# Performance work log

Hardware: AMD Instinct MI355X
Metric: run time of the kernel (lower is better)

The kernel has to match this reference:

```python
import jax, jax.numpy as jnp
import numpy as np

B, T_ENC, T_DEC = 16, 256, 64
N_MEL = 80
ENC_DIM = 512
ATTN_RNN_DIM = 1024
DEC_RNN_DIM = 1024
PRENET_DIM = 256
ATTN_DIM = 128
LOC_FILTERS = 32
LOC_KERNEL = 31


def setup_inputs() -> dict:
    key = jax.random.key(0)
    ks = jax.random.split(key, 32)
    s = 0.02
    inp = {
        "memory": jax.random.normal(ks[0], (B, T_ENC, ENC_DIM), jnp.float32),
        "decoder_inputs": jax.random.normal(ks[1], (B, N_MEL, T_DEC), jnp.float32),
        "memory_lengths": jax.random.randint(ks[2], (B,), T_ENC // 2, T_ENC + 1, jnp.int32),
        # prenet
        "prenet_W1": jax.random.normal(ks[3], (PRENET_DIM, N_MEL), jnp.float32) * s,
        "prenet_b1": jnp.zeros((PRENET_DIM,), jnp.float32),
        "prenet_W2": jax.random.normal(ks[4], (PRENET_DIM, PRENET_DIM), jnp.float32) * s,
        "prenet_b2": jnp.zeros((PRENET_DIM,), jnp.float32),
        # attention LSTMCell: input = prenet_dim + enc_dim
        "attn_rnn_Wih": jax.random.normal(ks[5], (4 * ATTN_RNN_DIM, PRENET_DIM + ENC_DIM), jnp.float32) * s,
        "attn_rnn_Whh": jax.random.normal(ks[6], (4 * ATTN_RNN_DIM, ATTN_RNN_DIM), jnp.float32) * s,
        "attn_rnn_bih": jnp.zeros((4 * ATTN_RNN_DIM,), jnp.float32),
        "attn_rnn_bhh": jnp.zeros((4 * ATTN_RNN_DIM,), jnp.float32),
        # attention projections (bias-free, Tacotron2 style)
        "query_W": jax.random.normal(ks[7], (ATTN_DIM, ATTN_RNN_DIM), jnp.float32) * s,
        "mem_W": jax.random.normal(ks[8], (ATTN_DIM, ENC_DIM), jnp.float32) * s,
        "loc_conv_W": jax.random.normal(ks[9], (LOC_FILTERS, 2, LOC_KERNEL), jnp.float32) * s,
        "loc_dense_W": jax.random.normal(ks[10], (ATTN_DIM, LOC_FILTERS), jnp.float32) * s,
        "attn_v": jax.random.normal(ks[11], (1, ATTN_DIM), jnp.float32) * s,
        # decoder LSTMCell: input = attn_rnn_dim + enc_dim
        "dec_rnn_Wih": jax.random.normal(ks[12], (4 * DEC_RNN_DIM, ATTN_RNN_DIM + ENC_DIM), jnp.float32) * s,
        "dec_rnn_Whh": jax.random.normal(ks[13], (4 * DEC_RNN_DIM, DEC_RNN_DIM), jnp.float32) * s,
        "dec_rnn_bih": jnp.zeros((4 * DEC_RNN_DIM,), jnp.float32),
        "dec_rnn_bhh": jnp.zeros((4 * DEC_RNN_DIM,), jnp.float32),
        # output heads
        "proj_W": jax.random.normal(ks[14], (N_MEL, DEC_RNN_DIM + ENC_DIM), jnp.float32) * s,
        "proj_b": jnp.zeros((N_MEL,), jnp.float32),
        "gate_W": jax.random.normal(ks[15], (1, DEC_RNN_DIM + ENC_DIM), jnp.float32) * s,
        "gate_b": jnp.zeros((1,), jnp.float32),
    }
    return inp


def _lstm_cell(x, h, c, Wih, Whh, bih, bhh):
    gates = x @ Wih.T + bih + h @ Whh.T + bhh  # [B, 4H]
    i, f, g, o = jnp.split(gates, 4, axis=-1)
    c2 = jax.nn.sigmoid(f) * c + jax.nn.sigmoid(i) * jnp.tanh(g)
    h2 = jax.nn.sigmoid(o) * jnp.tanh(c2)
    return h2, c2


def _decoder_forward(memory, decoder_inputs, memory_lengths,
                     prenet_W1, prenet_b1, prenet_W2, prenet_b2,
                     attn_rnn_Wih, attn_rnn_Whh, attn_rnn_bih, attn_rnn_bhh,
                     query_W, mem_W, loc_conv_W, loc_dense_W, attn_v,
                     dec_rnn_Wih, dec_rnn_Whh, dec_rnn_bih, dec_rnn_bhh,
                     proj_W, proj_b, gate_W, gate_b):
    b, t_enc, _ = memory.shape
    t_dec = decoder_inputs.shape[2]
    # parse_decoder_inputs: [B,80,T] -> [T,B,80]; prepend go frame
    frames = jnp.transpose(decoder_inputs, (2, 0, 1))  # [T,B,80]
    go = jnp.zeros((1, b, N_MEL), frames.dtype)
    frames = jnp.concatenate([go, frames], axis=0)  # [T+1,B,80]
    # prenet (dropout disabled for determinism)
    pre = jax.nn.relu(frames @ prenet_W1.T + prenet_b1)
    pre = jax.nn.relu(pre @ prenet_W2.T + prenet_b2)  # [T+1,B,256]
    pre = pre[:-1]  # steps use frames 0..T-1

    processed_memory = memory @ mem_W.T  # [B,T_enc,128]
    pad_mask = jnp.arange(t_enc)[None, :] >= memory_lengths[:, None]  # [B,T_enc] True=pad

    pad = (LOC_KERNEL - 1) // 2

    def step(carry, x_t):
        (ah, ac, dh, dc, aw, aw_cum, ctx) = carry
        cell_in = jnp.concatenate([x_t, ctx], axis=-1)
        ah, ac = _lstm_cell(cell_in, ah, ac, attn_rnn_Wih, attn_rnn_Whh, attn_rnn_bih, attn_rnn_bhh)
        # location-sensitive attention
        awc = jnp.stack([aw, aw_cum], axis=1)  # [B,2,T_enc]
        loc = jax.lax.conv_general_dilated(
            awc, loc_conv_W, window_strides=(1,), padding=[(pad, pad)],
            dimension_numbers=("NCH", "OIH", "NCH"))  # [B,32,T_enc]
        loc = jnp.transpose(loc, (0, 2, 1)) @ loc_dense_W.T  # [B,T_enc,128]
        query = (ah @ query_W.T)[:, None, :]  # [B,1,128]
        energies = jnp.squeeze(jnp.tanh(query + processed_memory + loc) @ attn_v.T, -1)  # [B,T_enc]
        energies = jnp.where(pad_mask, -1e9, energies)
        aw = jax.nn.softmax(energies, axis=1)
        ctx = jnp.einsum("bt,btd->bd", aw, memory)
        aw_cum = aw_cum + aw
        dec_in = jnp.concatenate([ah, ctx], axis=-1)
        dh, dc = _lstm_cell(dec_in, dh, dc, dec_rnn_Wih, dec_rnn_Whh, dec_rnn_bih, dec_rnn_bhh)
        dhc = jnp.concatenate([dh, ctx], axis=-1)
        mel = dhc @ proj_W.T + proj_b  # [B,80]
        gate = jnp.squeeze(dhc @ gate_W.T + gate_b, -1)  # [B]
        return (ah, ac, dh, dc, aw, aw_cum, ctx), (mel, gate, aw)

    z = jnp.zeros
    carry0 = (z((b, ATTN_RNN_DIM)), z((b, ATTN_RNN_DIM)),
              z((b, DEC_RNN_DIM)), z((b, DEC_RNN_DIM)),
              z((b, t_enc)), z((b, t_enc)), z((b, ENC_DIM)))
    _, (mels, gates, aligns) = jax.lax.scan(step, carry0, pre)
    # parse_decoder_outputs
    mel_outputs = jnp.transpose(mels, (1, 2, 0))  # [B,80,T_dec]
    gate_outputs = jnp.transpose(gates, (1, 0))  # [B,T_dec]
    alignments = jnp.transpose(aligns, (1, 0, 2))  # [B,T_dec,T_enc]
    return mel_outputs, gate_outputs, alignments


def reference(memory, decoder_inputs, memory_lengths,
              prenet_W1, prenet_b1, prenet_W2, prenet_b2,
              attn_rnn_Wih, attn_rnn_Whh, attn_rnn_bih, attn_rnn_bhh,
              query_W, mem_W, loc_conv_W, loc_dense_W, attn_v,
              dec_rnn_Wih, dec_rnn_Whh, dec_rnn_bih, dec_rnn_bhh,
              proj_W, proj_b, gate_W, gate_b):
    return _decoder_forward(memory, decoder_inputs, memory_lengths,
                            prenet_W1, prenet_b1, prenet_W2, prenet_b2,
                            attn_rnn_Wih, attn_rnn_Whh, attn_rnn_bih, attn_rnn_bhh,
                            query_W, mem_W, loc_conv_W, loc_dense_W, attn_v,
                            dec_rnn_Wih, dec_rnn_Whh, dec_rnn_bih, dec_rnn_bhh,
                            proj_W, proj_b, gate_W, gate_b)
```

## Files before the change

kernel.cpp:

```cpp
#include <hip/hip_runtime.h>

typedef __attribute__((ext_vector_type(8))) short short8;
typedef __attribute__((ext_vector_type(4))) float f32x4;
typedef unsigned short u16;
typedef unsigned int u32;
typedef unsigned long long u64;


static constexpr size_t OFF_WFA   = 0;
static constexpr size_t OFF_WFD   = 14680064;
static constexpr size_t OFF_PREF  = 35651584;
static constexpr size_t OFF_QWF   = 36175872;
static constexpr size_t OFF_MWT   = 36438016;
static constexpr size_t OFF_BA    = 36700160;
static constexpr size_t OFF_BD    = 36716544;
static constexpr size_t OFF_PM    = 36732928;
static constexpr size_t OFF_CTXF  = 38830080;
static constexpr size_t OFF_DHF   = 40960000;
static constexpr size_t OFF_AHFD  = 45219840;
static constexpr size_t OFF_CTXFD = 47349760;
static constexpr size_t OFF_DHFD  = 48414720;
static constexpr size_t OFF_BAR   = 50544640;
static constexpr size_t OFF_END   = 50548736;

__device__ __forceinline__ float sigmf(float x) { return 1.f / (1.f + expf(-x)); }
__device__ __forceinline__ float tanh_fast(float x) {
  float e2 = __expf(2.f * x);
  return 1.f - 2.f / (e2 + 1.f);
}
__device__ __forceinline__ u16 f2bf(float f) {
  u32 u = __float_as_uint(f);
  return (u16)((u + 0x7FFFu + ((u >> 16) & 1u)) >> 16);
}
__device__ __forceinline__ float bf2f(u16 x) { return __uint_as_float(((u32)x) << 16); }

__device__ __forceinline__ short8 ld_frag(const void* p) {
  return *(const short8*)p;
}
__device__ __forceinline__ short8 ld_frag_nt(const void* p) {
  const u64* q = (const u64*)p;
  u64 lo = __builtin_nontemporal_load(q);
  u64 hi = __builtin_nontemporal_load(q + 1);
  union { u64 q2[2]; short8 s; } u;
  u.q2[0] = lo; u.q2[1] = hi;
  return u.s;
}

__device__ __forceinline__ void st_u16_agent(u16* p, u16 v) {
  __hip_atomic_store(p, v, __ATOMIC_RELAXED, __HIP_MEMORY_SCOPE_AGENT);
}
__device__ __forceinline__ void st_f32_agent(float* p, float v) {
  __hip_atomic_store(p, v, __ATOMIC_RELAXED, __HIP_MEMORY_SCOPE_AGENT);
}
__device__ __forceinline__ void st_u64_agent(u64* p, u64 v) {
  __hip_atomic_store(p, v, __ATOMIC_RELAXED, __HIP_MEMORY_SCOPE_AGENT);
}
__device__ __forceinline__ u32 ld_u32_agent(const u32* p) {
  return __hip_atomic_load(p, __ATOMIC_RELAXED, __HIP_MEMORY_SCOPE_AGENT);
}
__device__ __forceinline__ void st_u32_agent(u32* p, u32 v) {
  __hip_atomic_store(p, v, __ATOMIC_RELAXED, __HIP_MEMORY_SCOPE_AGENT);
}

template <int SLP>
__device__ __forceinline__ void wait16(const u32* F, u32 target, int th) {
  if (th < 64) {
    const u32* pf = F + (th & 15) * 16;
    for (;;) {
      u32 v = ld_u32_agent(pf);
      if (__all(v >= target)) break;
      __builtin_amdgcn_s_sleep(SLP);
    }
  }
  __syncthreads();
}

__global__ void k_wfrag(const float* __restrict__ Wih, const float* __restrict__ Whh,
                        char* __restrict__ dst, int NT, int Kih) {
  int idx = blockIdx.x * 256 + threadIdx.x;
  int l = idx & 63;
  int st = idx >> 6;
  int s = st % NT, tile = st / NT;
  int r = l & 15, kg = l >> 4;
  int j = (r >> 2) * 1024 + tile * 4 + (r & 3);
  int k0 = s * 32 + kg * 8;
  const float* src = (k0 < Kih) ? (Wih + (size_t)j * Kih + k0)
                                : (Whh + (size_t)j * 1024 + (k0 - Kih));
  short8 v;
#pragma unroll
  for (int e = 0; e < 8; ++e) v[e] = (short)f2bf(src[e]);
  *(short8*)(dst + (size_t)idx * 16) = v;
}

__global__ void k_qwfrag(const float* __restrict__ qW, char* __restrict__ dst) {
  int idx = blockIdx.x * 256 + threadIdx.x;
  int l = idx & 63, tile = idx >> 6;
  int dt = tile >> 5, kt = tile & 31;
  int j = dt * 16 + (l & 15);
  int k0 = kt * 32 + (l >> 4) * 8;
  short8 v;
#pragma unroll
  for (int e = 0; e < 8; ++e) v[e] = (short)f2bf(qW[j * 1024 + k0 + e]);
  *(short8*)(dst + (size_t)idx * 16) = v;
}

__global__ void k_smallprep(const float* __restrict__ memW,
                            const float* __restrict__ abih, const float* __restrict__ abhh,
                            const float* __restrict__ dbih, const float* __restrict__ dbhh,
                            char* __restrict__ wsb) {
  int idx = blockIdx.x * 256 + threadIdx.x;
  if (idx < 65536) {
    int k = idx >> 7, d = idx & 127;
    ((float*)(wsb + OFF_MWT))[idx] = memW[d * 512 + k];
  } else if (idx < 69632) {
    int j = idx - 65536;
    ((float*)(wsb + OFF_BA))[j] = abih[j] + abhh[j];
  } else if (idx < 73728) {
    int j = idx - 69632;
    ((float*)(wsb + OFF_BD))[j] = dbih[j] + dbhh[j];
  }
}

__global__ void k_prenet(const float* __restrict__ dec_in,
                         const float* __restrict__ W1, const float* __restrict__ b1,
                         const float* __restrict__ W2, const float* __restrict__ b2,
                         char* __restrict__ wsb) {
  int s = blockIdx.x, b = blockIdx.y, th = threadIdx.x;
  __shared__ float frame[80];
  __shared__ float h1[256];
  if (th < 80) frame[th] = (s == 0) ? 0.f : dec_in[(b * 80 + th) * 64 + (s - 1)];
  __syncthreads();
  float a = b1[th];
  const float* w1r = W1 + th * 80;
  for (int m = 0; m < 80; ++m) a += w1r[m] * frame[m];
  h1[th] = fmaxf(a, 0.f);
  __syncthreads();
  float a2 = b2[th];
  const float* w2r = W2 + th * 256;
  for (int i = 0; i < 256; ++i) a2 += w2r[i] * h1[i];
  float pre = fmaxf(a2, 0.f);
  int k = th;
  ((u16*)(wsb + OFF_PREF))[(((size_t)s * 8 + (k >> 5)) * 64 + ((k >> 3) & 3) * 16 + b) * 8 + (k & 7)] = f2bf(pre);
}

__global__ void k_pm(const float* __restrict__ memory, char* __restrict__ wsb) {
  int bk = blockIdx.x, th = threadIdx.x;
  int b = bk >> 4, t0 = (bk & 15) * 16;
  __shared__ float mrow[16 * 512];
  for (int i = 0; i < 8; ++i) {
    int fi4 = i * 256 + th;
    int tl = fi4 >> 7, k4 = (fi4 & 127) << 2;
    *(float4*)&mrow[tl * 512 + k4] =
        *(const float4*)&memory[((size_t)(b * 256 + t0 + tl)) * 512 + k4];
  }
  __syncthreads();
  int d = th & 127, tl0 = th >> 7;
  float acc[8] = {};
  const float* mWT = (const float*)(wsb + OFF_MWT);
  float* pmw = (float*)(wsb + OFF_PM);
  for (int k = 0; k < 512; ++k) {
    float w = mWT[k * 128 + d];
#pragma unroll
    for (int i = 0; i < 8; ++i) acc[i] += w * mrow[(tl0 + i * 2) * 512 + k];
  }
  for (int i = 0; i < 8; ++i)
    pmw[((size_t)(b * 256 + t0 + tl0 + i * 2)) * 128 + d] = acc[i];
}

struct KParams {
  const float* memory;
  const int* mlen;
  const float* convW;
  const float* ldW;
  const float* attnv;
  const float* projW;
  const float* projb;
  const float* gateW;
  const float* gateb;
  char* wsb;
  float* out;
};

__global__ void __launch_bounds__(512, 1) k_main(KParams p) {
  const int th = threadIdx.x;
  const int bk = blockIdx.x;
  char* wsb = p.wsb;
  const int l = th & 63, w = th >> 6;
  u32* Af = (u32*)(wsb + OFF_BAR);
  u32* Df = (u32*)(wsb + OFF_BAR + 1024);
  u32* Bf = (u32*)(wsb + OFF_BAR + 2048);

  __shared__ float smC[4608];
  __shared__ float s2q[128], s2v[128];
  __shared__ u16 s_convF[8192];
  __shared__ u16 s_pack[512];
  __shared__ float s_e[256], s3wr[4];
  __shared__ float s1cw[1984];
  __shared__ float s_aw[256], s_awc[256];
  __shared__ float smW[4096];
  __shared__ u16 sp[1024];

  const float* pm = (const float*)(wsb + OFF_PM);

  if (bk < 16) {
    for (int i = th; i < 1984; i += 512) s1cw[i] = p.convW[i];
    for (int i = th; i < 4096; i += 512) ((u32*)s_convF)[i] = 0u;
    if (th < 128) s2v[th] = p.attnv[th];
    if (th < 256) { s_aw[th] = 0.f; s_awc[th] = 0.f; }
  }
  int lenB = 0;
  if (bk < 16) lenB = p.mlen[bk];

  short8 ldwB[8];
  if (bk < 16) {
    int kg = l >> 4, dcol = l & 15;
#pragma unroll
    for (int dt = 0; dt < 8; ++dt) {
      short8 v;
#pragma unroll
      for (int e = 0; e < 8; ++e)
        v[e] = (short)f2bf(p.ldW[(dt * 16 + dcol) * 32 + kg * 8 + e]);
      ldwB[dt] = v;
    }
  }
  __syncthreads();

  if (bk >= 16 && bk < 32) {
    const int i = bk - 16;
    const char* wfa = wsb + OFF_WFA;
    const int tI0 = i * 16 + w * 2;
    float bA[2][4], cA2[2] = {0.f, 0.f};
    {
      const float* ba = (const float*)(wsb + OFF_BA);
#pragma unroll
      for (int pq = 0; pq < 2; ++pq) {
        int idx = l * 2 + pq, lu = idx >> 4;
        int u = i * 64 + w * 8 + lu;
#pragma unroll
        for (int g = 0; g < 4; ++g) bA[pq][g] = ba[g * 1024 + u];
      }
    }
    f32x4 acc0, acc1;
    auto EARLY = [&](int t) {
      acc0 = f32x4{0.f, 0.f, 0.f, 0.f};
      acc1 = f32x4{0.f, 0.f, 0.f, 0.f};
      for (int e = 0; e < 40; ++e) {
        int s = (e < 8) ? e : (24 + (e - 8));
        const char* bsrc = (e < 8)
            ? wsb + OFF_PREF + (((size_t)t * 8 + s) * 64 + l) * 16
            : wsb + OFF_AHFD + (((size_t)t * 32 + (s - 24)) * 64 + l) * 16;
        short8 bv = ld_frag(bsrc);
        short8 a0 = *(const short8*)(wfa + (((size_t)tI0 * 56 + s) * 64 + l) * 16);
        short8 a1 = *(const short8*)(wfa + (((size_t)(tI0 + 1) * 56 + s) * 64 + l) * 16);
        acc0 = __builtin_amdgcn_mfma_f32_16x16x32_bf16(a0, bv, acc0, 0, 0, 0);
        acc1 = __builtin_amdgcn_mfma_f32_16x16x32_bf16(a1, bv, acc1, 0, 0, 0);
      }
    };
    EARLY(0);
    for (int t = 0; t < 64; ++t) {
      wait16<1>(Bf, (u32)t, th);
#pragma unroll
      for (int s = 8; s < 24; ++s) {
        short8 bv = ld_frag(wsb + OFF_CTXFD + (((size_t)t * 16 + (s - 8)) * 64 + l) * 16);
        short8 a0 = *(const short8*)(wfa + (((size_t)tI0 * 56 + s) * 64 + l) * 16);
        short8 a1 = *(const short8*)(wfa + (((size_t)(tI0 + 1) * 56 + s) * 64 + l) * 16);
        acc0 = __builtin_amdgcn_mfma_f32_16x16x32_bf16(a0, bv, acc0, 0, 0, 0);
        acc1 = __builtin_amdgcn_mfma_f32_16x16x32_bf16(a1, bv, acc1, 0, 0, 0);
      }
      {
        float* myW = smW + w * 512;
#pragma unroll
        for (int r4 = 0; r4 < 4; ++r4) {
          myW[((l >> 4) * 4 + r4) * 16 + (l & 15)] = acc0[r4];
          myW[256 + ((l >> 4) * 4 + r4) * 16 + (l & 15)] = acc1[r4];
        }
      }
      __syncthreads();
      {
        const float* myW = smW + w * 512;
        u16* myP = sp + w * 128;
#pragma unroll
        for (int pq = 0; pq < 2; ++pq) {
          int idx = l * 2 + pq, lu = idx >> 4, b = idx & 15;
          int rt = lu >> 2, uoff = lu & 3;
          float gi = myW[rt * 256 + (0 * 4 + uoff) * 16 + b] + bA[pq][0];
          float gf = myW[rt * 256 + (1 * 4 + uoff) * 16 + b] + bA[pq][1];
          float gg = myW[rt * 256 + (2 * 4 + uoff) * 16 + b] + bA[pq][2];
          float go = myW[rt * 256 + (3 * 4 + uoff) * 16 + b] + bA[pq][3];
          float c2 = sigmf(gf) * cA2[pq] + sigmf(gi) * tanhf(gg);
          float h2 = sigmf(go) * tanhf(c2);
          cA2[pq] = c2;
          myP[b * 8 + lu] = f2bf(h2);
        }
      }
      __syncthreads();
      if (l < 16) {
        const u64* src = (const u64*)(sp + w * 128) + l * 2;
        int slab = i * 8 + w;
        u64* dst = (u64*)(wsb + OFF_AHFD + ((size_t)(t + 1) * 32 + (slab >> 2)) * 1024 +
                          ((size_t)((slab & 3) * 16 + l)) * 16);
        st_u64_agent(dst, src[0]);
        st_u64_agent(dst + 1, src[1]);
      }
      __syncthreads();
      if (th == 0) st_u32_agent(Af + i * 16, (u32)(t + 1));
      if (t < 63) {
        wait16<1>(Af, (u32)(t + 1), th);
        EARLY(t + 1);
      }
    }
  } else if (bk >= 32 && bk < 48) {
    const int j = bk - 32;
    const char* wfd = wsb + OFF_WFD;
    const int tI0 = j * 16 + w * 2;
    float bD[2][4], cD2[2] = {0.f, 0.f};
    {
      const float* bd = (const float*)(wsb + OFF_BD);
#pragma unroll
      for (int pq = 0; pq < 2; ++pq) {
        int idx = l * 2 + pq, lu = idx >> 4;
        int u = j * 64 + w * 8 + lu;
#pragma unroll
        for (int g = 0; g < 4; ++g) bD[pq][g] = bd[g * 1024 + u];
      }
    }
    for (int t = 1; t <= 64; ++t) {
      wait16<2>(Af, (u32)t, th);
      wait16<2>(Bf, (u32)t, th);
      if (t >= 2) wait16<2>(Df, (u32)(t - 1), th);
      f32x4 acc0 = {0.f, 0.f, 0.f, 0.f}, acc1 = {0.f, 0.f, 0.f, 0.f};
      for (int s = 0; s < 80; ++s) {
        const char* bsrc;
        if (s < 32)      bsrc = wsb + OFF_AHFD + (((size_t)t * 32 + s) * 64 + l) * 16;
        else if (s < 48) bsrc = wsb + OFF_CTXFD + (((size_t)t * 16 + (s - 32)) * 64 + l) * 16;
        else             bsrc = wsb + OFF_DHFD + (((size_t)(t - 1) * 32 + (s - 48)) * 64 + l) * 16;
        short8 bv = ld_frag_nt(bsrc);
        short8 a0 = ld_frag_nt(wfd + (((size_t)tI0 * 80 + s) * 64 + l) * 16);
        short8 a1 = ld_frag_nt(wfd + (((size_t)(tI0 + 1) * 80 + s) * 64 + l) * 16);
        acc0 = __builtin_amdgcn_mfma_f32_16x16x32_bf16(a0, bv, acc0, 0, 0, 0);
        acc1 = __builtin_amdgcn_mfma_f32_16x16x32_bf16(a1, bv, acc1, 0, 0, 0);
      }
      {
        float* myW = smW + w * 512;
#pragma unroll
        for (int r4 = 0; r4 < 4; ++r4) {
          myW[((l >> 4) * 4 + r4) * 16 + (l & 15)] = acc0[r4];
          myW[256 + ((l >> 4) * 4 + r4) * 16 + (l & 15)] = acc1[r4];
        }
      }
      __syncthreads();
      {
        const float* myW = smW + w * 512;
        u16* myP = sp + w * 128;
        float* dhf = (float*)(wsb + OFF_DHF);
#pragma unroll
        for (int pq = 0; pq < 2; ++pq) {
          int idx = l * 2 + pq, lu = idx >> 4, b = idx & 15;
          int rt = lu >> 2, uoff = lu & 3;
          float gi = myW[rt * 256 + (0 * 4 + uoff) * 16 + b] + bD[pq][0];
          float gf = myW[rt * 256 + (1 * 4 + uoff) * 16 + b] + bD[pq][1];
          float gg = myW[rt * 256 + (2 * 4 + uoff) * 16 + b] + bD[pq][2];
          float go = myW[rt * 256 + (3 * 4 + uoff) * 16 + b] + bD[pq][3];
          float c2 = sigmf(gf) * cD2[pq] + sigmf(gi) * tanhf(gg);
          float h2 = sigmf(go) * tanhf(c2);
          cD2[pq] = c2;
          int u = j * 64 + w * 8 + lu;
          st_f32_agent(dhf + ((size_t)t * 1024 + u) * 16 + b, h2);
          myP[b * 8 + lu] = f2bf(h2);
        }
      }
      __syncthreads();
      if (l < 16) {
        const u64* src = (const u64*)(sp + w * 128) + l * 2;
        int slab = j * 8 + w;
        u64* dst = (u64*)(wsb + OFF_DHFD + ((size_t)t * 32 + (slab >> 2)) * 1024 +
                          ((size_t)((slab & 3) * 16 + l)) * 16);
        st_u64_agent(dst, src[0]);
        st_u64_agent(dst + 1, src[1]);
      }
      __syncthreads();
      if (th == 0) st_u32_agent(Df + j * 16, (u32)t);
    }
  } else if (bk < 16) {
    const int b = bk;
    for (int t = 0; t < 64; ++t) {
      {
        int jmax = (lenB + 15) >> 4;
        for (int jj = 0; jj < jmax; ++jj) {
          int idx = jj * 512 + th, tt = idx >> 5, f = idx & 31;
          float a = 0.f;
          const float* w0 = s1cw + f * 62;
#pragma unroll
          for (int kk = 0; kk < 31; ++kk) {
            int pos = tt + kk - 15;
            bool ok = (pos >= 0 && pos < 256);
            float awv = ok ? s_aw[pos] : 0.f;
            float awcv = ok ? s_awc[pos] : 0.f;
            a += awv * w0[kk] + awcv * w0[31 + kk];
          }
          s_convF[(tt >> 4) * 512 + ((f >> 3) * 16 + (tt & 15)) * 8 + (f & 7)] = f2bf(a);
        }
      }
      wait16<1>(Af, (u32)(t + 1), th);
      {
        f32x4 qacc = {0.f, 0.f, 0.f, 0.f};
        const char* qwf = wsb + OFF_QWF;
#pragma unroll 4
        for (int kt = 0; kt < 32; ++kt) {
          short8 av = *(const short8*)(qwf + (((size_t)w * 32 + kt) * 64 + l) * 16);
          short8 bv = ld_frag(wsb + OFF_AHFD + ((size_t)(t + 1) * 32 + kt) * 1024 +
                              ((size_t)(l >> 4) * 16 + b) * 16);
          qacc = __builtin_amdgcn_mfma_f32_16x16x32_bf16(av, bv, qacc, 0, 0, 0);
        }
        if ((l & 15) == 0) {
          int r0 = (l >> 4) * 4;
          s2q[w * 16 + r0]     = qacc[0];
          s2q[w * 16 + r0 + 1] = qacc[1];
          s2q[w * 16 + r0 + 2] = qacc[2];
          s2q[w * 16 + r0 + 3] = qacc[3];
        }
      }
      __syncthreads();
      {
#pragma unroll
        for (int tl = 0; tl < 2; ++tl) {
          int ttile = w * 2 + tl;
          short8 afc = *(const short8*)&s_convF[ttile * 512 + l * 8];
          int dcol = l & 15;
          float e0 = 0.f, e1 = 0.f, e2 = 0.f, e3 = 0.f;
          const float* pmb = pm + ((size_t)(b * 256 + ttile * 16 + (l >> 4) * 4)) * 128 + dcol;
#pragma unroll
          for (int dt = 0; dt < 8; ++dt) {
            f32x4 S = {0.f, 0.f, 0.f, 0.f};
            S = __builtin_amdgcn_mfma_f32_16x16x32_bf16(afc, ldwB[dt], S, 0, 0, 0);
            int d = dt * 16 + dcol;
            float qd = s2q[d], vd = s2v[d];
            e0 += vd * tanh_fast(qd + pmb[dt * 16 + 0 * 128] + S[0]);
            e1 += vd * tanh_fast(qd + pmb[dt * 16 + 1 * 128] + S[1]);
            e2 += vd * tanh_fast(qd + pmb[dt * 16 + 2 * 128] + S[2]);
            e3 += vd * tanh_fast(qd + pmb[dt * 16 + 3 * 128] + S[3]);
          }
#pragma unroll
          for (int off = 8; off; off >>= 1) {
            e0 += __shfl_xor(e0, off);
            e1 += __shfl_xor(e1, off);
            e2 += __shfl_xor(e2, off);
            e3 += __shfl_xor(e3, off);
          }
          if ((l & 15) == 0) {
            int tb0 = ttile * 16 + (l >> 4) * 4;
            s_e[tb0]     = (tb0     < lenB) ? __expf(e0) : 0.f;
            s_e[tb0 + 1] = (tb0 + 1 < lenB) ? __expf(e1) : 0.f;
            s_e[tb0 + 2] = (tb0 + 2 < lenB) ? __expf(e2) : 0.f;
            s_e[tb0 + 3] = (tb0 + 3 < lenB) ? __expf(e3) : 0.f;
          }
        }
      }
      __syncthreads();
      if (th < 256) {
        float v0 = s_e[th];
#pragma unroll
        for (int off = 32; off; off >>= 1) v0 += __shfl_xor(v0, off);
        if ((th & 63) == 0) s3wr[th >> 6] = v0;
      }
      __syncthreads();
      float rden = 1.f / (s3wr[0] + s3wr[1] + s3wr[2] + s3wr[3]);
      if (th < 256) {
        float a = s_e[th] * rden;
        s_aw[th] = a;
        s_awc[th] += a;
        p.out[82944 + ((size_t)(b * 64 + t)) * 256 + th] = a;
      }
      __syncthreads();
      {
        int dq = th & 127, tg = th >> 7;
        int d0 = dq * 4;
        float a0 = 0.f, a1 = 0.f, a2 = 0.f, a3 = 0.f;
        const float* mb = p.memory + ((size_t)b * 256) * 512 + d0;
        for (int tt = tg; tt < lenB; tt += 4) {
          float4 mv = *(const float4*)(mb + (size_t)tt * 512);
          float aw = s_aw[tt];
          a0 += aw * mv.x; a1 += aw * mv.y; a2 += aw * mv.z; a3 += aw * mv.w;
        }
        smC[tg * 512 + d0]     = a0;
        smC[tg * 512 + d0 + 1] = a1;
        smC[tg * 512 + d0 + 2] = a2;
        smC[tg * 512 + d0 + 3] = a3;
      }
      __syncthreads();
      {
        int d = th;
        float ctxv = smC[d] + smC[512 + d] + smC[1024 + d] + smC[1536 + d];
        st_f32_agent((float*)(wsb + OFF_CTXF) + (size_t)(t + 1) * 8192 + b * 512 + d, ctxv);
        s_pack[d] = f2bf(ctxv);
      }
      __syncthreads();
      if (th < 64) {
        u64 p0 = ((const u64*)s_pack)[th * 2];
        u64 p1 = ((const u64*)s_pack)[th * 2 + 1];
        u64* dst = (u64*)(wsb + OFF_CTXFD + ((size_t)(t + 1) * 16 + (th >> 2)) * 1024 +
                          ((size_t)(th & 3) * 16 + b) * 16);
        st_u64_agent(dst, p0);
        st_u64_agent(dst + 1, p1);
      }
      __syncthreads();
      if (th == 0) st_u32_agent(Bf + b * 16, (u32)(t + 1));
    }
  }

  if (bk >= 48) {
    wait16<64>(Df, 64u, th);
    wait16<64>(Bf, 64u, th);
  } else {
    wait16<4>(Df, 64u, th);
    wait16<4>(Bf, 64u, th);
  }
  {
    int t = bk & 63, pa = bk >> 6;
    const float* dh = (const float*)(wsb + OFF_DHF) + (size_t)(t + 1) * 16384;
    const float* cxt = (const float*)(wsb + OFF_CTXF) + (size_t)(t + 1) * 8192;
    int lim = (pa == 3) ? 336 : 320;
    for (int idx = th; idx < lim; idx += 512) {
      if (idx < 320) {
        int mi = idx >> 4, b = idx & 15, m = pa * 20 + mi;
        const float* wr = p.projW + (size_t)m * 1536;
        const float* cxb = cxt + b * 512;
        float a0 = 0.f, a1 = 0.f;
#pragma unroll 8
        for (int k = 0; k < 1024; k += 2) { a0 += wr[k] * dh[k * 16 + b]; a1 += wr[k + 1] * dh[(k + 1) * 16 + b]; }
#pragma unroll 8
        for (int k = 0; k < 512; k += 2)  { a0 += wr[1024 + k] * cxb[k]; a1 += wr[1025 + k] * cxb[k + 1]; }
        p.out[((size_t)(b * 80 + m)) * 64 + t] = a0 + a1 + p.projb[m];
      } else {
        int b = idx - 320;
        const float* cxb = cxt + b * 512;
        float a0 = 0.f, a1 = 0.f;
#pragma unroll 8
        for (int k = 0; k < 1024; k += 2) { a0 += p.gateW[k] * dh[k * 16 + b]; a1 += p.gateW[k + 1] * dh[(k + 1) * 16 + b]; }
#pragma unroll 8
        for (int k = 0; k < 512; k += 2)  { a0 += p.gateW[1024 + k] * cxb[k]; a1 += p.gateW[1025 + k] * cxb[k + 1]; }
        p.out[81920 + b * 64 + t] = a0 + a1 + p.gateb[0];
      }
    }
  }
}

extern "C" void kernel_launch(void* const* d_in, const int* in_sizes, int n_in,
                              void* d_out, int out_size, void* d_ws, size_t ws_size,
                              hipStream_t stream) {
  (void)in_sizes; (void)n_in; (void)out_size; (void)ws_size;
  const float* memory = (const float*)d_in[0];
  const float* dec_in = (const float*)d_in[1];
  const int*   mlen   = (const int*)d_in[2];
  const float* pW1    = (const float*)d_in[3];
  const float* pb1    = (const float*)d_in[4];
  const float* pW2    = (const float*)d_in[5];
  const float* pb2    = (const float*)d_in[6];
  const float* aWih   = (const float*)d_in[7];
  const float* aWhh   = (const float*)d_in[8];
  const float* abih   = (const float*)d_in[9];
  const float* abhh   = (const float*)d_in[10];
  const float* qW     = (const float*)d_in[11];
  const float* memW   = (const float*)d_in[12];
  const float* convW  = (const float*)d_in[13];
  const float* ldW    = (const float*)d_in[14];
  const float* attnv  = (const float*)d_in[15];
  const float* dWih   = (const float*)d_in[16];
  const float* dWhh   = (const float*)d_in[17];
  const float* dbih   = (const float*)d_in[18];
  const float* dbhh   = (const float*)d_in[19];
  const float* projW  = (const float*)d_in[20];
  const float* projb  = (const float*)d_in[21];
  const float* gateW  = (const float*)d_in[22];
  const float* gateb  = (const float*)d_in[23];
  char* wsb = (char*)d_ws;
  float* out = (float*)d_out;

  hipMemsetAsync(wsb + OFF_AHFD, 0, 32768, stream);
  hipMemsetAsync(wsb + OFF_CTXFD, 0, 16384, stream);
  hipMemsetAsync(wsb + OFF_DHFD, 0, 32768, stream);
  hipMemsetAsync(wsb + OFF_BAR, 0, 4096, stream);

  hipLaunchKernelGGL(k_wfrag, dim3(3584), dim3(256), 0, stream, aWih, aWhh, wsb + OFF_WFA, 56, 768);
  hipLaunchKernelGGL(k_wfrag, dim3(5120), dim3(256), 0, stream, dWih, dWhh, wsb + OFF_WFD, 80, 1536);
  hipLaunchKernelGGL(k_qwfrag, dim3(64), dim3(256), 0, stream, qW, wsb + OFF_QWF);
  hipLaunchKernelGGL(k_smallprep, dim3(288), dim3(256), 0, stream, memW, abih, abhh, dbih, dbhh, wsb);
  hipLaunchKernelGGL(k_prenet, dim3(64, 16), dim3(256), 0, stream, dec_in, pW1, pb1, pW2, pb2, wsb);
  hipLaunchKernelGGL(k_pm, dim3(256), dim3(256), 0, stream, memory, wsb);

  KParams p{memory, mlen, convW, ldW, attnv, projW, projb, gateW, gateb, wsb, out};
  void* args[] = { &p };
  hipLaunchCooperativeKernel((void*)k_main, dim3(256), dim3(512), args, 0, stream);
}
```

Measured before the change: 3.180 ms.

## Spread LSTM cells over twice as many blocks with one MFMA tile per wave

The attention-LSTM and decoder-LSTM recurrences each move from 16 to 32 persistent blocks, with each wave owning a single 16-row weight tile instead of two. The barrier flag arrays are widened and waits over them become 32-flag polls. Block index ranges for the later stages shift to match, and the decoder's nontemporal loads become plain loads. The aim is to halve the serial per-step weight streaming and MFMA chain on each block, at the cost of more inter-block synchronization per timestep.

Result: faster. 2.879 ms (-9.4%).

```diff
diff --git a/kernel.cpp b/kernel.cpp
--- a/kernel.cpp
+++ b/kernel.cpp
@@ -21,7 +21,7 @@
 static constexpr size_t OFF_CTXFD = 47349760;
 static constexpr size_t OFF_DHFD  = 48414720;
 static constexpr size_t OFF_BAR   = 50544640;
-static constexpr size_t OFF_END   = 50548736;
+static constexpr size_t OFF_END   = 50552832;
 
 __device__ __forceinline__ float sigmf(float x) { return 1.f / (1.f + expf(-x)); }
 __device__ __forceinline__ float tanh_fast(float x) {
@@ -37,14 +37,6 @@
 __device__ __forceinline__ short8 ld_frag(const void* p) {
   return *(const short8*)p;
 }
-__device__ __forceinline__ short8 ld_frag_nt(const void* p) {
-  const u64* q = (const u64*)p;
-  u64 lo = __builtin_nontemporal_load(q);
-  u64 hi = __builtin_nontemporal_load(q + 1);
-  union { u64 q2[2]; short8 s; } u;
-  u.q2[0] = lo; u.q2[1] = hi;
-  return u.s;
-}
 
 __device__ __forceinline__ void st_u16_agent(u16* p, u16 v) {
   __hip_atomic_store(p, v, __ATOMIC_RELAXED, __HIP_MEMORY_SCOPE_AGENT);
@@ -66,6 +58,18 @@
 __device__ __forceinline__ void wait16(const u32* F, u32 target, int th) {
   if (th < 64) {
     const u32* pf = F + (th & 15) * 16;
+    for (;;) {
+      u32 v = ld_u32_agent(pf);
+      if (__all(v >= target)) break;
+      __builtin_amdgcn_s_sleep(SLP);
+    }
+  }
+  __syncthreads();
+}
+template <int SLP>
+__device__ __forceinline__ void wait32(const u32* F, u32 target, int th) {
+  if (th < 64) {
+    const u32* pf = F + (th & 31) * 16;
     for (;;) {
       u32 v = ld_u32_agent(pf);
       if (__all(v >= target)) break;
@@ -187,8 +191,8 @@
   char* wsb = p.wsb;
   const int l = th & 63, w = th >> 6;
   u32* Af = (u32*)(wsb + OFF_BAR);
-  u32* Df = (u32*)(wsb + OFF_BAR + 1024);
-  u32* Bf = (u32*)(wsb + OFF_BAR + 2048);
+  u32* Df = (u32*)(wsb + OFF_BAR + 2048);
+  u32* Bf = (u32*)(wsb + OFF_BAR + 4096);
 
   __shared__ float smC[4608];
   __shared__ float s2q[128], s2v[128];
@@ -197,8 +201,8 @@
   __shared__ float s_e[256], s3wr[4];
   __shared__ float s1cw[1984];
   __shared__ float s_aw[256], s_awc[256];
-  __shared__ float smW[4096];
-  __shared__ u16 sp[1024];
+  __shared__ float smW[2048];
+  __shared__ u16 sp[512];
 
   const float* pm = (const float*)(wsb + OFF_PM);
 
@@ -225,35 +229,29 @@
   }
   __syncthreads();
 
-  if (bk >= 16 && bk < 32) {
+  if (bk >= 16 && bk < 48) {
     const int i = bk - 16;
     const char* wfa = wsb + OFF_WFA;
-    const int tI0 = i * 16 + w * 2;
-    float bA[2][4], cA2[2] = {0.f, 0.f};
+    const int tI = i * 8 + w;
+    const int ul = l >> 4, b = l & 15;
+    float bA[4], cA = 0.f;
     {
       const float* ba = (const float*)(wsb + OFF_BA);
-#pragma unroll
-      for (int pq = 0; pq < 2; ++pq) {
-        int idx = l * 2 + pq, lu = idx >> 4;
-        int u = i * 64 + w * 8 + lu;
-#pragma unroll
-        for (int g = 0; g < 4; ++g) bA[pq][g] = ba[g * 1024 + u];
-      }
-    }
-    f32x4 acc0, acc1;
+      int u = tI * 4 + ul;
+#pragma unroll
+      for (int g = 0; g < 4; ++g) bA[g] = ba[g * 1024 + u];
+    }
+    f32x4 acc;
     auto EARLY = [&](int t) {
-      acc0 = f32x4{0.f, 0.f, 0.f, 0.f};
-      acc1 = f32x4{0.f, 0.f, 0.f, 0.f};
+      acc = f32x4{0.f, 0.f, 0.f, 0.f};
       for (int e = 0; e < 40; ++e) {
         int s = (e < 8) ? e : (24 + (e - 8));
         const char* bsrc = (e < 8)
             ? wsb + OFF_PREF + (((size_t)t * 8 + s) * 64 + l) * 16
             : wsb + OFF_AHFD + (((size_t)t * 32 + (s - 24)) * 64 + l) * 16;
         short8 bv = ld_frag(bsrc);
-        short8 a0 = *(const short8*)(wfa + (((size_t)tI0 * 56 + s) * 64 + l) * 16);
-        short8 a1 = *(const short8*)(wfa + (((size_t)(tI0 + 1) * 56 + s) * 64 + l) * 16);
-        acc0 = __builtin_amdgcn_mfma_f32_16x16x32_bf16(a0, bv, acc0, 0, 0, 0);
-        acc1 = __builtin_amdgcn_mfma_f32_16x16x32_bf16(a1, bv, acc1, 0, 0, 0);
+        short8 av = *(const short8*)(wfa + (((size_t)tI * 56 + s) * 64 + l) * 16);
+        acc = __builtin_amdgcn_mfma_f32_16x16x32_bf16(av, bv, acc, 0, 0, 0);
       }
     };
     EARLY(0);
@@ -262,121 +260,95 @@
 #pragma unroll
       for (int s = 8; s < 24; ++s) {
         short8 bv = ld_frag(wsb + OFF_CTXFD + (((size_t)t * 16 + (s - 8)) * 64 + l) * 16);
-        short8 a0 = *(const short8*)(wfa + (((size_t)tI0 * 56 + s) * 64 + l) * 16);
-        short8 a1 = *(const short8*)(wfa + (((size_t)(tI0 + 1) * 56 + s) * 64 + l) * 16);
-        acc0 = __builtin_amdgcn_mfma_f32_16x16x32_bf16(a0, bv, acc0, 0, 0, 0);
-        acc1 = __builtin_amdgcn_mfma_f32_16x16x32_bf16(a1, bv, acc1, 0, 0, 0);
-      }
-      {
-        float* myW = smW + w * 512;
-#pragma unroll
-        for (int r4 = 0; r4 < 4; ++r4) {
-          myW[((l >> 4) * 4 + r4) * 16 + (l & 15)] = acc0[r4];
-          myW[256 + ((l >> 4) * 4 + r4) * 16 + (l & 15)] = acc1[r4];
-        }
-      }
-      __syncthreads();
-      {
-        const float* myW = smW + w * 512;
-        u16* myP = sp + w * 128;
-#pragma unroll
-        for (int pq = 0; pq < 2; ++pq) {
-          int idx = l * 2 + pq, lu = idx >> 4, b = idx & 15;
-          int rt = lu >> 2, uoff = lu & 3;
-          float gi = myW[rt * 256 + (0 * 4 + uoff) * 16 + b] + bA[pq][0];
-          float gf = myW[rt * 256 + (1 * 4 + uoff) * 16 + b] + bA[pq][1];
-          float gg = myW[rt * 256 + (2 * 4 + uoff) * 16 + b] + bA[pq][2];
-          float go = myW[rt * 256 + (3 * 4 + uoff) * 16 + b] + bA[pq][3];
-          float c2 = sigmf(gf) * cA2[pq] + sigmf(gi) * tanhf(gg);
-          float h2 = sigmf(go) * tanhf(c2);
-          cA2[pq] = c2;
-          myP[b * 8 + lu] = f2bf(h2);
-        }
+        short8 av = *(const short8*)(wfa + (((size_t)tI * 56 + s) * 64 + l) * 16);
+        acc = __builtin_amdgcn_mfma_f32_16x16x32_bf16(av, bv, acc, 0, 0, 0);
+      }
+      {
+        float* myW = smW + w * 256;
+#pragma unroll
+        for (int r4 = 0; r4 < 4; ++r4)
+          myW[((l >> 4) * 4 + r4) * 16 + (l & 15)] = acc[r4];
+      }
+      __syncthreads();
+      {
+        const float* myW = smW + w * 256;
+        u16* myP = sp + w * 64;
+        float gi = myW[(0 * 4 + ul) * 16 + b] + bA[0];
+        float gf = myW[(1 * 4 + ul) * 16 + b] + bA[1];
+        float gg = myW[(2 * 4 + ul) * 16 + b] + bA[2];
+        float go = myW[(3 * 4 + ul) * 16 + b] + bA[3];
+        float c2 = sigmf(gf) * cA + sigmf(gi) * tanhf(gg);
+        float h2 = sigmf(go) * tanhf(c2);
+        cA = c2;
+        myP[b * 4 + ul] = f2bf(h2);
       }
       __syncthreads();
       if (l < 16) {
-        const u64* src = (const u64*)(sp + w * 128) + l * 2;
-        int slab = i * 8 + w;
-        u64* dst = (u64*)(wsb + OFF_AHFD + ((size_t)(t + 1) * 32 + (slab >> 2)) * 1024 +
-                          ((size_t)((slab & 3) * 16 + l)) * 16);
-        st_u64_agent(dst, src[0]);
-        st_u64_agent(dst + 1, src[1]);
+        u64 val = ((const u64*)(sp + w * 64))[l];
+        u64* dst = (u64*)(wsb + OFF_AHFD + ((size_t)(t + 1) * 32 + (tI >> 3)) * 1024 +
+                          ((size_t)(((tI >> 1) & 3) * 16 + l)) * 16 + (size_t)(tI & 1) * 8);
+        st_u64_agent(dst, val);
       }
       __syncthreads();
       if (th == 0) st_u32_agent(Af + i * 16, (u32)(t + 1));
       if (t < 63) {
-        wait16<1>(Af, (u32)(t + 1), th);
+        wait32<1>(Af, (u32)(t + 1), th);
         EARLY(t + 1);
       }
     }
-  } else if (bk >= 32 && bk < 48) {
-    const int j = bk - 32;
+  } else if (bk >= 48 && bk < 80) {
+    const int j = bk - 48;
     const char* wfd = wsb + OFF_WFD;
-    const int tI0 = j * 16 + w * 2;
-    float bD[2][4], cD2[2] = {0.f, 0.f};
+    const int tI = j * 8 + w;
+    const int ul = l >> 4, b = l & 15;
+    float bD[4], cD = 0.f;
     {
       const float* bd = (const float*)(wsb + OFF_BD);
-#pragma unroll
-      for (int pq = 0; pq < 2; ++pq) {
-        int idx = l * 2 + pq, lu = idx >> 4;
-        int u = j * 64 + w * 8 + lu;
-#pragma unroll
-        for (int g = 0; g < 4; ++g) bD[pq][g] = bd[g * 1024 + u];
-      }
+      int u = tI * 4 + ul;
+#pragma unroll
+      for (int g = 0; g < 4; ++g) bD[g] = bd[g * 1024 + u];
     }
     for (int t = 1; t <= 64; ++t) {
-      wait16<2>(Af, (u32)t, th);
+      wait32<2>(Af, (u32)t, th);
       wait16<2>(Bf, (u32)t, th);
-      if (t >= 2) wait16<2>(Df, (u32)(t - 1), th);
-      f32x4 acc0 = {0.f, 0.f, 0.f, 0.f}, acc1 = {0.f, 0.f, 0.f, 0.f};
+      if (t >= 2) wait32<2>(Df, (u32)(t - 1), th);
+      f32x4 acc = {0.f, 0.f, 0.f, 0.f};
       for (int s = 0; s < 80; ++s) {
         const char* bsrc;
         if (s < 32)      bsrc = wsb + OFF_AHFD + (((size_t)t * 32 + s) * 64 + l) * 16;
         else if (s < 48) bsrc = wsb + OFF_CTXFD + (((size_t)t * 16 + (s - 32)) * 64 + l) * 16;
         else             bsrc = wsb + OFF_DHFD + (((size_t)(t - 1) * 32 + (s - 48)) * 64 + l) * 16;
-        short8 bv = ld_frag_nt(bsrc);
-        short8 a0 = ld_frag_nt(wfd + (((size_t)tI0 * 80 + s) * 64 + l) * 16);
-        short8 a1 = ld_frag_nt(wfd + (((size_t)(tI0 + 1) * 80 + s) * 64 + l) * 16);
-        acc0 = __builtin_amdgcn_mfma_f32_16x16x32_bf16(a0, bv, acc0, 0, 0, 0);
-        acc1 = __builtin_amdgcn_mfma_f32_16x16x32_bf16(a1, bv, acc1, 0, 0, 0);
-      }
-      {
-        float* myW = smW + w * 512;
-#pragma unroll
-        for (int r4 = 0; r4 < 4; ++r4) {
-          myW[((l >> 4) * 4 + r4) * 16 + (l & 15)] = acc0[r4];
-          myW[256 + ((l >> 4) * 4 + r4) * 16 + (l & 15)] = acc1[r4];
-        }
-      }
-      __syncthreads();
-      {
-        const float* myW = smW + w * 512;
-        u16* myP = sp + w * 128;
-        float* dhf = (float*)(wsb + OFF_DHF);
-#pragma unroll
-        for (int pq = 0; pq < 2; ++pq) {
-          int idx = l * 2 + pq, lu = idx >> 4, b = idx & 15;
-          int rt = lu >> 2, uoff = lu & 3;
-          float gi = myW[rt * 256 + (0 * 4 + uoff) * 16 + b] + bD[pq][0];
-          float gf = myW[rt * 256 + (1 * 4 + uoff) * 16 + b] + bD[pq][1];
-          float gg = myW[rt * 256 + (2 * 4 + uoff) * 16 + b] + bD[pq][2];
-          float go = myW[rt * 256 + (3 * 4 + uoff) * 16 + b] + bD[pq][3];
-          float c2 = sigmf(gf) * cD2[pq] + sigmf(gi) * tanhf(gg);
-          float h2 = sigmf(go) * tanhf(c2);
-          cD2[pq] = c2;
-          int u = j * 64 + w * 8 + lu;
-          st_f32_agent(dhf + ((size_t)t * 1024 + u) * 16 + b, h2);
-          myP[b * 8 + lu] = f2bf(h2);
-        }
+        short8 bv = ld_frag(bsrc);
+        short8 av = *(const short8*)(wfd + (((size_t)tI * 80 + s) * 64 + l) * 16);
+        acc = __builtin_amdgcn_mfma_f32_16x16x32_bf16(av, bv, acc, 0, 0, 0);
+      }
+      {
+        float* myW = smW + w * 256;
+#pragma unroll
+        for (int r4 = 0; r4 < 4; ++r4)
+          myW[((l >> 4) * 4 + r4) * 16 + (l & 15)] = acc[r4];
+      }
+      __syncthreads();
+      {
+        const float* myW = smW + w * 256;
+        u16* myP = sp + w * 64;
+        float gi = myW[(0 * 4 + ul) * 16 + b] + bD[0];
+        float gf = myW[(1 * 4 + ul) * 16 + b] + bD[1];
+        float gg = myW[(2 * 4 + ul) * 16 + b] + bD[2];
+        float go = myW[(3 * 4 + ul) * 16 + b] + bD[3];
+        float c2 = sigmf(gf) * cD + sigmf(gi) * tanhf(gg);
+        float h2 = sigmf(go) * tanhf(c2);
+        cD = c2;
+        int u = tI * 4 + ul;
+        st_f32_agent((float*)(wsb + OFF_DHF) + ((size_t)t * 1024 + u) * 16 + b, h2);
+        myP[b * 4 + ul] = f2bf(h2);
       }
       __syncthreads();
       if (l < 16) {
-        const u64* src = (const u64*)(sp + w * 128) + l * 2;
-        int slab = j * 8 + w;
-        u64* dst = (u64*)(wsb + OFF_DHFD + ((size_t)t * 32 + (slab >> 2)) * 1024 +
-                          ((size_t)((slab & 3) * 16 + l)) * 16);
-        st_u64_agent(dst, src[0]);
-        st_u64_agent(dst + 1, src[1]);
+        u64 val = ((const u64*)(sp + w * 64))[l];
+        u64* dst = (u64*)(wsb + OFF_DHFD + ((size_t)t * 32 + (tI >> 3)) * 1024 +
+                          ((size_t)(((tI >> 1) & 3) * 16 + l)) * 16 + (size_t)(tI & 1) * 8);
+        st_u64_agent(dst, val);
       }
       __syncthreads();
       if (th == 0) st_u32_agent(Df + j * 16, (u32)t);
@@ -401,7 +373,7 @@
           s_convF[(tt >> 4) * 512 + ((f >> 3) * 16 + (tt & 15)) * 8 + (f & 7)] = f2bf(a);
         }
       }
-      wait16<1>(Af, (u32)(t + 1), th);
+      wait32<1>(Af, (u32)(t + 1), th);
       {
         f32x4 qacc = {0.f, 0.f, 0.f, 0.f};
         const char* qwf = wsb + OFF_QWF;
@@ -508,11 +480,11 @@
     }
   }
 
-  if (bk >= 48) {
-    wait16<64>(Df, 64u, th);
+  if (bk >= 80) {
+    wait32<64>(Df, 64u, th);
     wait16<64>(Bf, 64u, th);
   } else {
-    wait16<4>(Df, 64u, th);
+    wait32<4>(Df, 64u, th);
     wait16<4>(Bf, 64u, th);
   }
   {
@@ -579,7 +551,7 @@
   hipMemsetAsync(wsb + OFF_AHFD, 0, 32768, stream);
   hipMemsetAsync(wsb + OFF_CTXFD, 0, 16384, stream);
   hipMemsetAsync(wsb + OFF_DHFD, 0, 32768, stream);
-  hipMemsetAsync(wsb + OFF_BAR, 0, 4096, stream);
+  hipMemsetAsync(wsb + OFF_BAR, 0, 8192, stream);
 
   hipLaunchKernelGGL(k_wfrag, dim3(3584), dim3(256), 0, stream, aWih, aWhh, wsb + OFF_WFA, 56, 768);
   hipLaunchKernelGGL(k_wfrag, dim3(5120), dim3(256), 0, stream, dWih, dWhh, wsb + OFF_WFD, 80, 1536);
```
